# Optimization experiments

Hardware: AMD Instinct MI355X
Metric: run time of the kernel (lower is better)

## Reference

```python
import jax, jax.numpy as jnp
import numpy as np

B, T, I, H, L, C = 64, 2048, 256, 256, 2, 10


def _lstm_layer(xs, W_ih, W_hh, b_ih, b_hh):
    """xs: [B, T, in]; returns hidden sequence [B, T, H]. PyTorch gate order i,f,g,o."""
    # Precompute input contribution for all timesteps in one big GEMM.
    gx = jnp.einsum('bti,gi->btg', xs, W_ih) + b_ih + b_hh  # [B, T, 4H]
    gx = jnp.transpose(gx, (1, 0, 2))  # [T, B, 4H]
    Hh = W_hh.shape[1]
    h0 = jnp.zeros((xs.shape[0], Hh), xs.dtype)
    c0 = jnp.zeros((xs.shape[0], Hh), xs.dtype)

    def step(carry, g_t):
        h, c = carry
        g = g_t + h @ W_hh.T  # [B, 4H]
        i, f, gg, o = jnp.split(g, 4, axis=-1)
        i = jax.nn.sigmoid(i)
        f = jax.nn.sigmoid(f)
        gg = jnp.tanh(gg)
        o = jax.nn.sigmoid(o)
        c = f * c + i * gg
        h = o * jnp.tanh(c)
        return (h, c), h

    (_, _), hs = jax.lax.scan(step, (h0, c0), gx)  # hs: [T, B, H]
    return jnp.transpose(hs, (1, 0, 2))


def setup_inputs() -> dict:
    key = jax.random.key(0)
    ks = jax.random.split(key, 11)
    s_i = 1.0 / np.sqrt(H)
    inp = {
        'x': jax.random.normal(ks[0], (B, T, I), jnp.float32),
        'W_ih_0': jax.random.uniform(ks[1], (4 * H, I), jnp.float32, -s_i, s_i),
        'W_hh_0': jax.random.uniform(ks[2], (4 * H, H), jnp.float32, -s_i, s_i),
        'b_ih_0': jax.random.uniform(ks[3], (4 * H,), jnp.float32, -s_i, s_i),
        'b_hh_0': jax.random.uniform(ks[4], (4 * H,), jnp.float32, -s_i, s_i),
        'W_ih_1': jax.random.uniform(ks[5], (4 * H, H), jnp.float32, -s_i, s_i),
        'W_hh_1': jax.random.uniform(ks[6], (4 * H, H), jnp.float32, -s_i, s_i),
        'b_ih_1': jax.random.uniform(ks[7], (4 * H,), jnp.float32, -s_i, s_i),
        'b_hh_1': jax.random.uniform(ks[8], (4 * H,), jnp.float32, -s_i, s_i),
        'W_fc': jax.random.uniform(ks[9], (C, H), jnp.float32, -s_i, s_i),
        'b_fc': jax.random.uniform(ks[10], (C,), jnp.float32, -s_i, s_i),
    }
    return inp


def reference(x, W_ih_0, W_hh_0, b_ih_0, b_hh_0, W_ih_1, W_hh_1, b_ih_1, b_hh_1, W_fc, b_fc):
    h1 = _lstm_layer(x, W_ih_0, W_hh_0, b_ih_0, b_hh_0)   # [B, T, H]
    h2 = _lstm_layer(h1, W_ih_1, W_hh_1, b_ih_1, b_hh_1)  # [B, T, H]
    out = h2[:, -1, :] @ W_fc.T + b_fc                     # [B, C]
    return out
```

## Files before the change

kernel.cpp:

```cpp
#include <hip/hip_runtime.h>
#include <hip/hip_bf16.h>

#define BB 64
#define TT 2048
#define HH 256
#define H4 1024
#define NC 10
#define CH 32
#define NCH (TT / CH)
#define NR 4

typedef _Float16 half2v __attribute__((ext_vector_type(2)));
typedef _Float16 half8  __attribute__((ext_vector_type(8)));
typedef float    f32x4  __attribute__((ext_vector_type(4)));

struct __align__(128) Line { unsigned v; unsigned pad[31]; };

__device__ __forceinline__ float fsig_(float x) {
    return __fdividef(1.f, 1.f + __expf(-x));
}
__device__ __forceinline__ float ftanh_(float x) {
    return 1.f - __fdividef(2.f, __expf(2.f * x) + 1.f);
}

__device__ __forceinline__ float fdot2_(unsigned wu, half2v hv, float acc) {
#if __has_builtin(__builtin_amdgcn_fdot2)
    return __builtin_amdgcn_fdot2(__builtin_bit_cast(half2v, wu), hv, acc, false);
#else
    half2v w = __builtin_bit_cast(half2v, wu);
    return acc + (float)w[0] * (float)hv[0] + (float)w[1] * (float)hv[1];
#endif
}

__device__ __forceinline__ void wait_flags(Line* f, unsigned target, int tid) {
    if (tid < 64) {
        while (true) {
            unsigned v = __hip_atomic_load(&f[tid].v, __ATOMIC_RELAXED,
                                           __HIP_MEMORY_SCOPE_AGENT);
            if (__all(v >= target)) break;
            __builtin_amdgcn_s_sleep(2);
        }
        if (tid == 0)
            __builtin_amdgcn_fence(__ATOMIC_ACQUIRE, "agent");
    }
    __syncthreads();
}

__global__ void f32_to_f16(const float* __restrict__ in,
                           _Float16* __restrict__ out, int n8)
{
    int i = blockIdx.x * 256 + threadIdx.x;
    if (i >= n8) return;
    float4 v0 = ((const float4*)in)[2 * i];
    float4 v1 = ((const float4*)in)[2 * i + 1];
    half8 h;
    h[0] = (_Float16)v0.x; h[1] = (_Float16)v0.y;
    h[2] = (_Float16)v0.z; h[3] = (_Float16)v0.w;
    h[4] = (_Float16)v1.x; h[5] = (_Float16)v1.y;
    h[6] = (_Float16)v1.z; h[7] = (_Float16)v1.w;
    ((half8*)out)[i] = h;
}

__global__ void prep_w(const float* __restrict__ W, uint4* __restrict__ out)
{
    const int k2 = blockIdx.x, t = threadIdx.x;
    unsigned q4[4];
#pragma unroll
    for (int q = 0; q < 4; q++) {
        const float* wr = W + (size_t)(q * 256 + t) * 256 + 2 * k2;
        union { _Float16 h[2]; unsigned u; } cv;
        cv.h[0] = (_Float16)wr[0];
        cv.h[1] = (_Float16)wr[1];
        q4[q] = cv.u;
    }
    out[(size_t)k2 * 256 + t] = make_uint4(q4[0], q4[1], q4[2], q4[3]);
}

__global__ __launch_bounds__(512, 1)
void lstm_pipe(const _Float16* __restrict__ x16,
               const _Float16* __restrict__ w16a, const _Float16* __restrict__ w16b,
               const float* __restrict__ bih0, const float* __restrict__ bhh0,
               const float* __restrict__ bih1, const float* __restrict__ bhh1,
               const uint4* __restrict__ wpk0, const uint4* __restrict__ wpk1,
               _Float16* __restrict__ gx1r, _Float16* __restrict__ gx2r,
               _Float16* __restrict__ h1c,
               float* __restrict__ hs1, float* __restrict__ cs1,
               float* __restrict__ hs2, float* __restrict__ cs2,
               Line* __restrict__ fG1, Line* __restrict__ fL1,
               Line* __restrict__ fG2, Line* __restrict__ fL2)
{
    __shared__ __align__(16) unsigned char pool[1088 + 4096 + 32 * 4096];
    _Float16* hlb = (_Float16*)pool;
    float*    pre = (float*)(pool + 1088);
    uint4*    wl  = (uint4*)(pool + 1088 + 4096);

    const int wg = blockIdx.x, tid = threadIdx.x;
    const int role = wg >> 6, sub = wg & 63;

    if (role == 1 || role == 2) {
        const bool isG2 = (role == 2);
        const _Float16* A  = isG2 ? h1c  : x16;
        const _Float16* Wm = isG2 ? w16b : w16a;
        const float* b1 = isG2 ? bih1 : bih0;
        const float* b2 = isG2 ? bhh1 : bhh0;
        _Float16* outr  = isG2 ? gx2r : gx1r;
        Line* fOut      = isG2 ? fG2  : fG1;

        const int v = tid >> 6, lane = tid & 63;
        const int lrow = lane & 15, lkg = lane >> 4;
        const int rquad = v & 3, nqh = v >> 2;
        const int tcl = sub & 31;
        const int n0 = (sub >> 5) * 512 + nqh * 256;

        const _Float16* wrow0 = Wm + (size_t)(n0 + lrow) * 256 + lkg * 8;

        for (int c = 0; c < NCH; c++) {
            if (isG2) {
                wait_flags(fL1, (unsigned)(c + 1), tid);
                if (c >= NR) wait_flags(fL2, (unsigned)(c - (NR - 1)), tid);
            } else {
                if (c >= NR) wait_flags(fL1, (unsigned)(c - (NR - 1)), tid);
            }
            const int tc = c * CH + tcl;
            const int slot = c % NR;
            const _Float16* arow =
                A + ((size_t)(rquad * 16 + lrow) * TT + tc) * 256 + lkg * 8;

            f32x4 acc[16];
#pragma unroll
            for (int j = 0; j < 16; j++) acc[j] = (f32x4)(0.f);
#pragma unroll
            for (int k0 = 0; k0 < 256; k0 += 32) {
                half8 a = *(const half8*)(arow + k0);
#pragma unroll
                for (int j = 0; j < 16; j++) {
                    half8 bf = *(const half8*)(wrow0 + (size_t)j * 16 * 256 + k0);
                    acc[j] = __builtin_amdgcn_mfma_f32_16x16x32_f16(a, bf, acc[j], 0, 0, 0);
                }
            }
            const int bout = rquad * 16 + lkg * 4;
#pragma unroll
            for (int j = 0; j < 16; j++) {
                int n = n0 + j * 16 + lrow;
                float bsum = b1[n] + b2[n];
                int u = n & 255, q = n >> 8;
#pragma unroll
                for (int r = 0; r < 4; r++) {
                    outr[((size_t)(slot * CH + tcl) * BB + bout + r) * H4 + u * 4 + q] =
                        (_Float16)(acc[j][r] + bsum);
                }
            }
            __syncthreads();
            if (tid == 0) {
                __builtin_amdgcn_fence(__ATOMIC_RELEASE, "agent");
                __hip_atomic_store(&fOut[sub].v, (unsigned)(c + 1),
                                   __ATOMIC_RELAXED, __HIP_MEMORY_SCOPE_AGENT);
            }
        }
        return;
    }

    const bool isL2 = (role == 3);
    const uint4* wpk = isL2 ? wpk1 : wpk0;
    const _Float16* gxr = isL2 ? gx2r : gx1r;
    float* hst = isL2 ? hs2 : hs1;
    float* cst = isL2 ? cs2 : cs1;
    Line* fIn  = isL2 ? fG2 : fG1;
    Line* fOut = isL2 ? fL2 : fL1;
    const int b = sub;
    const int tau = tid & 255, hh = tid >> 8;

#pragma unroll
    for (int m = 0; m < 16; m++) {
        int e = m * 512 + tid;
        int s = e >> 8, tp = e & 255;
        int k2g = (s < 16) ? (48 + s) : (96 + s);
        wl[e] = wpk[(size_t)k2g * 256 + tp];
    }

    uint4 w4[48];
    {
        const volatile unsigned* wv = (const volatile unsigned*)wpk;
#pragma unroll
        for (int r = 0; r < 48; r++) {
            size_t base = ((size_t)(hh * 64 + r) * 256 + tau) * 4;
            w4[r].x = wv[base + 0];
            w4[r].y = wv[base + 1];
            w4[r].z = wv[base + 2];
            w4[r].w = wv[base + 3];
        }
    }

    const uint4* wbase = wl + hh * 4096 + tau;

    float c_ = 0.f, lastH = 0.f;
    if (hh == 0) {
        c_ = cst[b * HH + tau];
        lastH = hst[b * HH + tau];
        hlb[tau] = (_Float16)lastH;
    }
    __syncthreads();

    int p = 0;
    for (int ch = 0; ch < NCH; ch++) {
        wait_flags(fIn, (unsigned)(ch + 1), tid);
        const _Float16* gsl = gxr + (size_t)(ch % NR) * CH * BB * H4
                            + (size_t)b * H4 + tau * 4;
        uint2 gq = make_uint2(0, 0);
        if (hh == 1) gq = *(const uint2*)gsl;

        for (int l = 0; l < CH; l++) {
            uint2 gqn = make_uint2(0, 0);
            if (hh == 1 && l < CH - 1)
                gqn = *(const uint2*)(gsl + (size_t)(l + 1) * BB * H4);

            const uint4* hp4 = (const uint4*)(hlb + p * 272) + hh * 16;
            float a0 = 0.f, a1 = 0.f, a2 = 0.f, a3 = 0.f;

#pragma unroll
            for (int j = 0; j < 12; j++) {
                uint4 hq = hp4[j];
#pragma unroll
                for (int u = 0; u < 4; u++) {
                    half2v hv = __builtin_bit_cast(half2v, hq[u]);
                    uint4 w = w4[4 * j + u];
                    a0 = fdot2_(w.x, hv, a0);
                    a1 = fdot2_(w.y, hv, a1);
                    a2 = fdot2_(w.z, hv, a2);
                    a3 = fdot2_(w.w, hv, a3);
                }
            }
#pragma unroll
            for (int j = 12; j < 16; j++) {
                uint4 hq = hp4[j];
#pragma unroll
                for (int u = 0; u < 4; u++) {
                    uint4 w = wbase[(4 * (j - 12) + u) * 256];
                    half2v hv = __builtin_bit_cast(half2v, hq[u]);
                    a0 = fdot2_(w.x, hv, a0);
                    a1 = fdot2_(w.y, hv, a1);
                    a2 = fdot2_(w.z, hv, a2);
                    a3 = fdot2_(w.w, hv, a3);
                }
            }

            if (hh == 1) {
                half2v glo = __builtin_bit_cast(half2v, gq.x);
                half2v ghi = __builtin_bit_cast(half2v, gq.y);
                float4 vv = make_float4(a0 + (float)glo[0], a1 + (float)glo[1],
                                        a2 + (float)ghi[0], a3 + (float)ghi[1]);
                *(float4*)&pre[tau * 4] = vv;
            }
            __syncthreads();

            if (hh == 0) {
                float4 po = *(const float4*)&pre[tau * 4];
                float ig = fsig_(a0 + po.x);
                float fg = fsig_(a1 + po.y);
                float gg = ftanh_(a2 + po.z);
                float og = fsig_(a3 + po.w);
                c_ = fg * c_ + ig * gg;
                float h = og * ftanh_(c_);
                lastH = h;
                if (!isL2) {
                    int tc = ch * CH + l;
                    h1c[((size_t)b * TT + tc) * HH + tau] = (_Float16)h;
                }
                hlb[(p ^ 1) * 272 + tau] = (_Float16)h;
            }
            __syncthreads();
            p ^= 1;
            gq = gqn;
        }

        if (tid == 0) {
            if (!isL2) __builtin_amdgcn_fence(__ATOMIC_RELEASE, "agent");
            __hip_atomic_store(&fOut[b].v, (unsigned)(ch + 1),
                               __ATOMIC_RELAXED, __HIP_MEMORY_SCOPE_AGENT);
        }
    }

    if (hh == 0) {
        cst[b * HH + tau] = c_;
        hst[b * HH + tau] = lastH;
    }
}

__global__ void fc_kernel(const float* __restrict__ h2,
                          const float* __restrict__ Wfc,
                          const float* __restrict__ bfc,
                          float* __restrict__ out)
{
    __shared__ float hs[256];
    int b = blockIdx.x, tid = threadIdx.x;
    hs[tid] = h2[b * HH + tid];
    __syncthreads();
    if (tid < NC) {
        float s = bfc[tid];
        for (int k = 0; k < 256; k++) s += hs[k] * Wfc[tid * 256 + k];
        out[b * NC + tid] = s;
    }
}

extern "C" void kernel_launch(void* const* d_in, const int* in_sizes, int n_in,
                              void* d_out, int out_size, void* d_ws, size_t ws_size,
                              hipStream_t stream)
{
    const float* x    = (const float*)d_in[0];
    const float* Wih0 = (const float*)d_in[1];
    const float* Whh0 = (const float*)d_in[2];
    const float* bih0 = (const float*)d_in[3];
    const float* bhh0 = (const float*)d_in[4];
    const float* Wih1 = (const float*)d_in[5];
    const float* Whh1 = (const float*)d_in[6];
    const float* bih1 = (const float*)d_in[7];
    const float* bhh1 = (const float*)d_in[8];
    const float* Wfc  = (const float*)d_in[9];
    const float* bfc  = (const float*)d_in[10];

    const size_t x16_b  = (size_t)BB * TT * HH * 2;
    const size_t h1c_b  = x16_b;
    const size_t gxr_b  = (size_t)NR * CH * BB * H4 * 2;
    const size_t w16_b  = (size_t)H4 * HH * 2;
    const size_t wpk_b  = (size_t)128 * 256 * 16;
    const size_t st_b   = (size_t)4 * BB * HH * 4;

    char* pp = (char*)d_ws;
    _Float16* x16  = (_Float16*)pp;  pp += x16_b;
    _Float16* h1c  = (_Float16*)pp;  pp += h1c_b;
    _Float16* gx1r = (_Float16*)pp;  pp += gxr_b;
    _Float16* gx2r = (_Float16*)pp;  pp += gxr_b;
    _Float16* w16a = (_Float16*)pp;  pp += w16_b;
    _Float16* w16b = (_Float16*)pp;  pp += w16_b;
    uint4*    wpk0 = (uint4*)pp;     pp += wpk_b;
    uint4*    wpk1 = (uint4*)pp;     pp += wpk_b;
    float*    hs1  = (float*)pp;
    float*    cs1  = hs1 + BB * HH;
    float*    hs2  = cs1 + BB * HH;
    float*    cs2  = hs2 + BB * HH;
    pp += st_b;
    Line* fG1 = (Line*)pp;
    Line* fL1 = fG1 + 64;
    Line* fG2 = fL1 + 64;
    Line* fL2 = fG2 + 64;

    hipMemsetAsync(hs1, 0, st_b + 256 * sizeof(Line), stream);

    prep_w<<<128, 256, 0, stream>>>(Whh0, wpk0);
    prep_w<<<128, 256, 0, stream>>>(Whh1, wpk1);
    f32_to_f16<<<(BB * TT * HH / 8 + 255) / 256, 256, 0, stream>>>(x, x16, BB * TT * HH / 8);
    f32_to_f16<<<(H4 * HH / 8 + 255) / 256, 256, 0, stream>>>(Wih0, w16a, H4 * HH / 8);
    f32_to_f16<<<(H4 * HH / 8 + 255) / 256, 256, 0, stream>>>(Wih1, w16b, H4 * HH / 8);

    lstm_pipe<<<256, 512, 0, stream>>>(x16, w16a, w16b,
                                       bih0, bhh0, bih1, bhh1,
                                       wpk0, wpk1, gx1r, gx2r, h1c,
                                       hs1, cs1, hs2, cs2,
                                       fG1, fL1, fG2, fL2);

    fc_kernel<<<BB, 256, 0, stream>>>(hs2, Wfc, bfc, (float*)d_out);
}
```

Before: 3.491 ms.

## Use one thread per hidden unit in recurrent LSTM blocks, dropping split-K reduction

The recurrent workgroups shrink from 512 to 256 threads, and each thread now computes the full 256-long dot product for its hidden unit. Three quarters of the packed recurrent weights live in registers (96 uint4) and the rest in LDS. This removes the cross-half partial-sum exchange through shared memory and one barrier per timestep. The GEMM producer blocks also drop to 4 waves, each doing two passes over the N dimension. In exchange, per-thread work and register pressure double, which risks spilling and a longer serial FMA chain per step.

```diff
diff --git a/kernel.cpp b/kernel.cpp
--- a/kernel.cpp
+++ b/kernel.cpp
@@ -76,7 +76,7 @@
     out[(size_t)k2 * 256 + t] = make_uint4(q4[0], q4[1], q4[2], q4[3]);
 }
 
-__global__ __launch_bounds__(512, 1)
+__global__ __launch_bounds__(256, 1)
 void lstm_pipe(const _Float16* __restrict__ x16,
                const _Float16* __restrict__ w16a, const _Float16* __restrict__ w16b,
                const float* __restrict__ bih0, const float* __restrict__ bhh0,
@@ -89,10 +89,9 @@
                Line* __restrict__ fG1, Line* __restrict__ fL1,
                Line* __restrict__ fG2, Line* __restrict__ fL2)
 {
-    __shared__ __align__(16) unsigned char pool[1088 + 4096 + 32 * 4096];
+    __shared__ __align__(16) unsigned char pool[1088 + 32 * 4096];
     _Float16* hlb = (_Float16*)pool;
-    float*    pre = (float*)(pool + 1088);
-    uint4*    wl  = (uint4*)(pool + 1088 + 4096);
+    uint4*    wl  = (uint4*)(pool + 1088);
 
     const int wg = blockIdx.x, tid = threadIdx.x;
     const int role = wg >> 6, sub = wg & 63;
@@ -108,11 +107,7 @@
 
         const int v = tid >> 6, lane = tid & 63;
         const int lrow = lane & 15, lkg = lane >> 4;
-        const int rquad = v & 3, nqh = v >> 2;
-        const int tcl = sub & 31;
-        const int n0 = (sub >> 5) * 512 + nqh * 256;
-
-        const _Float16* wrow0 = Wm + (size_t)(n0 + lrow) * 256 + lkg * 8;
+        const int tcl = sub & 31, nhalf = sub >> 5;
 
         for (int c = 0; c < NCH; c++) {
             if (isG2) {
@@ -124,30 +119,35 @@
             const int tc = c * CH + tcl;
             const int slot = c % NR;
             const _Float16* arow =
-                A + ((size_t)(rquad * 16 + lrow) * TT + tc) * 256 + lkg * 8;
-
-            f32x4 acc[16];
-#pragma unroll
-            for (int j = 0; j < 16; j++) acc[j] = (f32x4)(0.f);
-#pragma unroll
-            for (int k0 = 0; k0 < 256; k0 += 32) {
-                half8 a = *(const half8*)(arow + k0);
+                A + ((size_t)(v * 16 + lrow) * TT + tc) * 256 + lkg * 8;
+            const int bout = v * 16 + lkg * 4;
+
+#pragma unroll
+            for (int pass = 0; pass < 2; pass++) {
+                const int n0 = nhalf * 512 + pass * 256;
+                const _Float16* wrow = Wm + (size_t)(n0 + lrow) * 256 + lkg * 8;
+                f32x4 acc[16];
+#pragma unroll
+                for (int j = 0; j < 16; j++) acc[j] = (f32x4)(0.f);
+#pragma unroll
+                for (int k0 = 0; k0 < 256; k0 += 32) {
+                    half8 a = *(const half8*)(arow + k0);
+#pragma unroll
+                    for (int j = 0; j < 16; j++) {
+                        half8 bf = *(const half8*)(wrow + (size_t)j * 16 * 256 + k0);
+                        acc[j] = __builtin_amdgcn_mfma_f32_16x16x32_f16(a, bf, acc[j], 0, 0, 0);
+                    }
+                }
 #pragma unroll
                 for (int j = 0; j < 16; j++) {
-                    half8 bf = *(const half8*)(wrow0 + (size_t)j * 16 * 256 + k0);
-                    acc[j] = __builtin_amdgcn_mfma_f32_16x16x32_f16(a, bf, acc[j], 0, 0, 0);
-                }
-            }
-            const int bout = rquad * 16 + lkg * 4;
-#pragma unroll
-            for (int j = 0; j < 16; j++) {
-                int n = n0 + j * 16 + lrow;
-                float bsum = b1[n] + b2[n];
-                int u = n & 255, q = n >> 8;
-#pragma unroll
-                for (int r = 0; r < 4; r++) {
-                    outr[((size_t)(slot * CH + tcl) * BB + bout + r) * H4 + u * 4 + q] =
-                        (_Float16)(acc[j][r] + bsum);
+                    int n = n0 + j * 16 + lrow;
+                    float bsum = b1[n] + b2[n];
+                    int u = n & 255, q = n >> 8;
+#pragma unroll
+                    for (int r = 0; r < 4; r++) {
+                        outr[((size_t)(slot * CH + tcl) * BB + bout + r) * H4 + u * 4 + q] =
+                            (_Float16)(acc[j][r] + bsum);
+                    }
                 }
             }
             __syncthreads();
@@ -168,22 +168,18 @@
     Line* fIn  = isL2 ? fG2 : fG1;
     Line* fOut = isL2 ? fL2 : fL1;
     const int b = sub;
-    const int tau = tid & 255, hh = tid >> 8;
-
-#pragma unroll
-    for (int m = 0; m < 16; m++) {
-        int e = m * 512 + tid;
-        int s = e >> 8, tp = e & 255;
-        int k2g = (s < 16) ? (48 + s) : (96 + s);
-        wl[e] = wpk[(size_t)k2g * 256 + tp];
-    }
-
-    uint4 w4[48];
+    const int tau = tid;
+
+#pragma unroll
+    for (int m = 0; m < 32; m++)
+        wl[m * 256 + tau] = wpk[(size_t)(96 + m) * 256 + tau];
+
+    uint4 w4[96];
     {
         const volatile unsigned* wv = (const volatile unsigned*)wpk;
 #pragma unroll
-        for (int r = 0; r < 48; r++) {
-            size_t base = ((size_t)(hh * 64 + r) * 256 + tau) * 4;
+        for (int r = 0; r < 96; r++) {
+            size_t base = ((size_t)r * 256 + tau) * 4;
             w4[r].x = wv[base + 0];
             w4[r].y = wv[base + 1];
             w4[r].z = wv[base + 2];
@@ -191,14 +187,9 @@
         }
     }
 
-    const uint4* wbase = wl + hh * 4096 + tau;
-
-    float c_ = 0.f, lastH = 0.f;
-    if (hh == 0) {
-        c_ = cst[b * HH + tau];
-        lastH = hst[b * HH + tau];
-        hlb[tau] = (_Float16)lastH;
-    }
+    float c_ = cst[b * HH + tau];
+    float lastH = hst[b * HH + tau];
+    hlb[tau] = (_Float16)lastH;
     __syncthreads();
 
     int p = 0;
@@ -206,19 +197,18 @@
         wait_flags(fIn, (unsigned)(ch + 1), tid);
         const _Float16* gsl = gxr + (size_t)(ch % NR) * CH * BB * H4
                             + (size_t)b * H4 + tau * 4;
-        uint2 gq = make_uint2(0, 0);
-        if (hh == 1) gq = *(const uint2*)gsl;
+        uint2 gq = *(const uint2*)gsl;
 
         for (int l = 0; l < CH; l++) {
-            uint2 gqn = make_uint2(0, 0);
-            if (hh == 1 && l < CH - 1)
+            uint2 gqn = gq;
+            if (l < CH - 1)
                 gqn = *(const uint2*)(gsl + (size_t)(l + 1) * BB * H4);
 
-            const uint4* hp4 = (const uint4*)(hlb + p * 272) + hh * 16;
+            const uint4* hp4 = (const uint4*)(hlb + p * 272);
             float a0 = 0.f, a1 = 0.f, a2 = 0.f, a3 = 0.f;
 
 #pragma unroll
-            for (int j = 0; j < 12; j++) {
+            for (int j = 0; j < 24; j++) {
                 uint4 hq = hp4[j];
 #pragma unroll
                 for (int u = 0; u < 4; u++) {
@@ -231,11 +221,11 @@
                 }
             }
 #pragma unroll
-            for (int j = 12; j < 16; j++) {
+            for (int j = 24; j < 32; j++) {
                 uint4 hq = hp4[j];
 #pragma unroll
                 for (int u = 0; u < 4; u++) {
-                    uint4 w = wbase[(4 * (j - 12) + u) * 256];
+                    uint4 w = wl[(4 * (j - 24) + u) * 256 + tau];
                     half2v hv = __builtin_bit_cast(half2v, hq[u]);
                     a0 = fdot2_(w.x, hv, a0);
                     a1 = fdot2_(w.y, hv, a1);
@@ -244,30 +234,18 @@
                 }
             }
 
-            if (hh == 1) {
-                half2v glo = __builtin_bit_cast(half2v, gq.x);
-                half2v ghi = __builtin_bit_cast(half2v, gq.y);
-                float4 vv = make_float4(a0 + (float)glo[0], a1 + (float)glo[1],
-                                        a2 + (float)ghi[0], a3 + (float)ghi[1]);
-                *(float4*)&pre[tau * 4] = vv;
-            }
-            __syncthreads();
-
-            if (hh == 0) {
-                float4 po = *(const float4*)&pre[tau * 4];
-                float ig = fsig_(a0 + po.x);
-                float fg = fsig_(a1 + po.y);
-                float gg = ftanh_(a2 + po.z);
-                float og = fsig_(a3 + po.w);
-                c_ = fg * c_ + ig * gg;
-                float h = og * ftanh_(c_);
-                lastH = h;
-                if (!isL2) {
-                    int tc = ch * CH + l;
-                    h1c[((size_t)b * TT + tc) * HH + tau] = (_Float16)h;
-                }
-                hlb[(p ^ 1) * 272 + tau] = (_Float16)h;
-            }
+            half2v glo = __builtin_bit_cast(half2v, gq.x);
+            half2v ghi = __builtin_bit_cast(half2v, gq.y);
+            float ig = fsig_(a0 + (float)glo[0]);
+            float fg = fsig_(a1 + (float)glo[1]);
+            float gg = ftanh_(a2 + (float)ghi[0]);
+            float og = fsig_(a3 + (float)ghi[1]);
+            c_ = fg * c_ + ig * gg;
+            float h = og * ftanh_(c_);
+            lastH = h;
+            if (!isL2)
+                h1c[((size_t)b * TT + ch * CH + l) * HH + tau] = (_Float16)h;
+            hlb[(p ^ 1) * 272 + tau] = (_Float16)h;
             __syncthreads();
             p ^= 1;
             gq = gqn;
@@ -280,10 +258,8 @@
         }
     }
 
-    if (hh == 0) {
-        cst[b * HH + tau] = c_;
-        hst[b * HH + tau] = lastH;
-    }
+    cst[b * HH + tau] = c_;
+    hst[b * HH + tau] = lastH;
 }
 
 __global__ void fc_kernel(const float* __restrict__ h2,
@@ -352,7 +328,7 @@
     f32_to_f16<<<(H4 * HH / 8 + 255) / 256, 256, 0, stream>>>(Wih0, w16a, H4 * HH / 8);
     f32_to_f16<<<(H4 * HH / 8 + 255) / 256, 256, 0, stream>>>(Wih1, w16b, H4 * HH / 8);
 
-    lstm_pipe<<<256, 512, 0, stream>>>(x16, w16a, w16b,
+    lstm_pipe<<<256, 256, 0, stream>>>(x16, w16a, w16b,
                                        bih0, bhh0, bih1, bhh1,
                                        wpk0, wpk1, gx1r, gx2r, h1c,
                                        hs1, cs1, hs2, cs2,
```

New measurement: 6.973 ms. +99.7%, slower.
